# Kernel optimization log

Hardware: AMD Instinct MI355X
Metric: run time of the kernel (lower is better)

The kernel has to match this reference:

```python
import jax, jax.numpy as jnp
import numpy as np

B, S, F_IN = 8, 4096, 256      # batch, frames, mel bins
C = 256                        # model_complexity (out_features of attention)
G = 8                          # n_heads (groups)
K = 31                         # w_size (local window, odd)
F_OUT = 88                     # output_features (piano keys)
PAD = (K - 1) // 2


def setup_inputs() -> dict:
    key = jax.random.key(0)
    ks = jax.random.split(key, 7)
    s = 0.05
    return {
        "spec": jax.random.normal(ks[0], (B, S, F_IN), jnp.float32),
        "W_q": jax.random.normal(ks[1], (F_IN, C), jnp.float32) * s,
        "W_k": jax.random.normal(ks[2], (F_IN, C), jnp.float32) * s,
        "W_v": jax.random.normal(ks[3], (F_IN, C), jnp.float32) * s,
        "rel": jax.random.normal(ks[4], (C, K), jnp.float32),
        "W_lin": jax.random.normal(ks[5], (C, F_OUT), jnp.float32) * s,
        "b_lin": jax.random.normal(ks[6], (F_OUT,), jnp.float32) * s,
    }


def reference(spec, W_q, W_k, W_v, rel, W_lin, b_lin):
    b, s, _ = spec.shape
    d = C // G  # per-head dim
    # QKV projections (no bias, as in the module)
    q = spec @ W_q                                             # [B,S,C]
    padded = jnp.pad(spec, ((0, 0), (PAD, PAD), (0, 0)))       # [B,S+2p,F]
    k = padded @ W_k                                           # [B,S+2p,C]
    v = padded @ W_v
    # unfold: window index [S,K]
    idx = jnp.arange(s)[:, None] + jnp.arange(K)[None, :]      # [S,K]
    kw = jnp.transpose(k[:, idx, :], (0, 1, 3, 2))             # [B,S,C,K]
    vw = jnp.transpose(v[:, idx, :], (0, 1, 3, 2))             # [B,S,C,K]
    kw = kw + rel                                              # positional bias [C,K]
    kw = kw.reshape(b, s, G, d, K)
    vw = vw.reshape(b, s, G, d, K)
    qh = q.reshape(b, s, G, d)
    energy = jnp.einsum('bsgd,bsgdk->bsgk', qh, kw)            # [B,S,G,K]
    attn = jax.nn.softmax(energy, axis=-1)                     # [B,S,G,K]
    out = jnp.einsum('bsgk,bsgdk->bsgd', attn, vw).reshape(b, s, C)
    frame_pred = jax.nn.sigmoid(out @ W_lin + b_lin)           # [B,S,F_OUT]
    return frame_pred, attn
```

## Files before the change

kernel.cpp:

```cpp
#include <hip/hip_runtime.h>
#include <hip/hip_bf16.h>
#include <math.h>

#define B_   8
#define S_   4096
#define FIN  256
#define C_   256
#define G_   8
#define D_   32
#define K_   31
#define PAD_ 15
#define FOUT 88

typedef __bf16 bf16;
typedef __attribute__((ext_vector_type(8))) __bf16 bf16x8;
typedef __attribute__((ext_vector_type(4))) __bf16 bf16x4;
typedef __attribute__((ext_vector_type(4))) float f32x4;

#define MFMA16(A, B, C) __builtin_amdgcn_mfma_f32_16x16x32_bf16(A, B, C, 0, 0, 0)

__global__ __launch_bounds__(256) void split_spec(
    const float* __restrict__ spec, bf16* __restrict__ sh, bf16* __restrict__ sl)
{
    const size_t base = ((size_t)blockIdx.x * 256 + threadIdx.x) * 8;
    float4 x0 = *(const float4*)&spec[base];
    float4 x1 = *(const float4*)&spec[base + 4];
    float xs[8] = {x0.x, x0.y, x0.z, x0.w, x1.x, x1.y, x1.z, x1.w};
    bf16x8 H, L;
#pragma unroll
    for (int j = 0; j < 8; ++j) {
        bf16 h = (bf16)xs[j];
        H[j] = h;
        L[j] = (bf16)(xs[j] - (float)h);
    }
    *(bf16x8*)&sh[base] = H;
    *(bf16x8*)&sl[base] = L;
}

__global__ void split_w(const float* __restrict__ Wq, const float* __restrict__ Wk,
                        const float* __restrict__ Wv,
                        bf16* __restrict__ bth, bf16* __restrict__ btl)
{
    const int k = blockIdx.x;
    const int w = blockIdx.y;
    const int n = threadIdx.x;
    const float* W = (w == 0) ? Wq : (w == 1) ? Wk : Wv;
    float x = W[(size_t)k * 256 + n];
    bf16 h = (bf16)x;
    bf16 l = (bf16)(x - (float)h);
    size_t o = (size_t)w * 65536 + (size_t)n * 256 + k;
    bth[o] = h;
    btl[o] = l;
}

__global__ void split_wl(const float* __restrict__ Wl,
                         bf16* __restrict__ wlh, bf16* __restrict__ wll)
{
    const int k = blockIdx.x;
    const int n = threadIdx.x;
    const float x = (n < FOUT) ? Wl[(size_t)k * FOUT + n] : 0.f;
    bf16 h = (bf16)x;
    bf16 l = (bf16)(x - (float)h);
    wlh[(size_t)n * 256 + k] = h;
    wll[(size_t)n * 256 + k] = l;
}

__global__ void vt_pad(bf16* __restrict__ Vt) {
    const int idx = blockIdx.x * 256 + threadIdx.x;
    const int bd  = idx >> 4;
    const int pos = (idx & 15) * 4;
    const int off = (pos < 16) ? pos : 4096 + pos;
    bf16x4 z = {};
    *(bf16x4*)&Vt[(size_t)bd * 4160 + off] = z;
}

__global__ void rel_prep(const float* __restrict__ rel,
                         bf16* __restrict__ relH, bf16* __restrict__ relL) {
    const int idx = blockIdx.x * 256 + threadIdx.x;
    const int g = idx >> 10, k = (idx >> 5) & 31, d = idx & 31;
    const float v = (k < 31) ? rel[(size_t)(g * 32 + d) * 31 + k] : 0.f;
    bf16 h = (bf16)v;
    relH[idx] = h;
    relL[idx] = (bf16)(v - (float)h);
}

__device__ __forceinline__ void gload16(const bf16* g, bf16* l) {
    __builtin_amdgcn_global_load_lds(
        (const __attribute__((address_space(1))) void*)g,
        (__attribute__((address_space(3))) void*)l, 16, 0, 0);
}

__device__ __forceinline__ void stage_tile(const bf16* g, bf16* l, int t) {
    const int lg = ((t & 3) ^ ((t >> 3) & 3)) * 8;
    const int r0 = t >> 2;
    const int r1 = 64 + (t >> 2);
    const int u0 = (t & ~63) * 8;
    gload16(g + (size_t)r0 * 256 + lg, l + u0);
    gload16(g + (size_t)r1 * 256 + lg, l + u0 + 2048);
}

__device__ __forceinline__ bf16x8 frag_ld(const bf16* l, int r, int cl) {
    return *(const bf16x8*)&l[r * 32 + ((cl ^ ((r >> 1) & 3)) << 3)];
}

__global__ __launch_bounds__(256) void qkv_mfma(
    const bf16* __restrict__ sh, const bf16* __restrict__ sl,
    const bf16* __restrict__ bth, const bf16* __restrict__ btl,
    bf16* __restrict__ Qh, bf16* __restrict__ Ql,
    bf16* __restrict__ Kh, bf16* __restrict__ Kl,
    bf16* __restrict__ Vt)
{
    __shared__ bf16 lds[2 * 4 * 4096];

    const int t   = threadIdx.x;
    const int swz = ((blockIdx.x & 7) * 192) + (blockIdx.x >> 3);
    const int mt  = swz / 6, nt = swz % 6;
    const int wt  = nt >> 1;
    const int m0  = mt * 128, n0 = (nt & 1) * 128;
    const bool three = (wt < 2);

    const bf16* ah_g = sh  + (size_t)m0 * 256;
    const bf16* al_g = sl  + (size_t)m0 * 256;
    const bf16* bh_g = bth + (size_t)wt * 65536 + (size_t)n0 * 256;
    const bf16* bl_g = btl + (size_t)wt * 65536 + (size_t)n0 * 256;

    const int lane = t & 63, wid = t >> 6;
    const int wr = (wid >> 1) * 64, wc = (wid & 1) * 64;
    const int fr = lane & 15, cl = lane >> 4;

    f32x4 acc[4][4];
#pragma unroll
    for (int m = 0; m < 4; ++m)
#pragma unroll
        for (int n = 0; n < 4; ++n)
            acc[m][n] = (f32x4){0.f, 0.f, 0.f, 0.f};

    stage_tile(ah_g, lds, t);
    if (three) stage_tile(al_g, lds + 4096, t);
    stage_tile(bh_g, lds + 8192, t);
    stage_tile(bl_g, lds + 12288, t);
    __syncthreads();

    for (int ks = 0; ks < 8; ++ks) {
        const int cur = (ks & 1) * 16384;
        if (ks < 7) {
            const int nxt = 16384 - cur;
            const int ko  = (ks + 1) * 32;
            stage_tile(ah_g + ko, lds + nxt, t);
            if (three) stage_tile(al_g + ko, lds + nxt + 4096, t);
            stage_tile(bh_g + ko, lds + nxt + 8192, t);
            stage_tile(bl_g + ko, lds + nxt + 12288, t);
        }

        bf16x8 ah[4], bh[4], bl[4];
#pragma unroll
        for (int m = 0; m < 4; ++m) ah[m] = frag_ld(lds + cur, wr + m * 16 + fr, cl);
#pragma unroll
        for (int n = 0; n < 4; ++n) {
            bh[n] = frag_ld(lds + cur + 8192,  wc + n * 16 + fr, cl);
            bl[n] = frag_ld(lds + cur + 12288, wc + n * 16 + fr, cl);
        }
#pragma unroll
        for (int m = 0; m < 4; ++m)
#pragma unroll
            for (int n = 0; n < 4; ++n) {
                acc[m][n] = MFMA16(ah[m], bh[n], acc[m][n]);
                acc[m][n] = MFMA16(ah[m], bl[n], acc[m][n]);
            }
        if (three) {
            bf16x8 al[4];
#pragma unroll
            for (int m = 0; m < 4; ++m) al[m] = frag_ld(lds + cur + 4096, wr + m * 16 + fr, cl);
#pragma unroll
            for (int m = 0; m < 4; ++m)
#pragma unroll
                for (int n = 0; n < 4; ++n)
                    acc[m][n] = MFMA16(al[m], bh[n], acc[m][n]);
        }
        __syncthreads();
    }

    if (wt < 2) {
        bf16* Oh = (wt == 0) ? Qh : Kh;
        bf16* Ol = (wt == 0) ? Ql : Kl;
#pragma unroll
        for (int m = 0; m < 4; ++m) {
            const int gr = m0 + wr + m * 16 + cl * 4;
#pragma unroll
            for (int n = 0; n < 4; ++n) {
                const int gc = n0 + wc + n * 16 + fr;
#pragma unroll
                for (int i = 0; i < 4; ++i) {
                    const float v = acc[m][n][i];
                    const bf16 hh = (bf16)v;
                    const size_t off = (size_t)(gr + i) * 256 + gc;
                    Oh[off] = hh;
                    Ol[off] = (bf16)(v - (float)hh);
                }
            }
        }
    } else {
#pragma unroll
        for (int m = 0; m < 4; ++m) {
            const int gr = m0 + wr + m * 16 + cl * 4;
            const int bb = gr >> 12, sr = gr & 4095;
#pragma unroll
            for (int n = 0; n < 4; ++n) {
                const int gc = n0 + wc + n * 16 + fr;
                bf16x4 pk;
#pragma unroll
                for (int i = 0; i < 4; ++i) pk[i] = (bf16)acc[m][n][i];
                *(bf16x4*)&Vt[(size_t)(bb * 256 + gc) * 4160 + 16 + sr] = pk;
            }
        }
    }
}

__global__ __launch_bounds__(256) void attn_mfma(
    const bf16* __restrict__ Qh, const bf16* __restrict__ Ql,
    const bf16* __restrict__ Kh, const bf16* __restrict__ Kl,
    const bf16* __restrict__ Vt,
    const bf16* __restrict__ relH, const bf16* __restrict__ relL,
    float* __restrict__ attn, bf16* __restrict__ Obf)
{
    __shared__ char ldsb[18432];

    const int t    = threadIdx.x;
    const int wid  = t >> 6;
    const int lane = t & 63;
    const int fr   = lane & 15;
    const int q    = lane >> 4;
    const int f7   = fr & 7;
    const int sl   = lane >> 2;
    const int jj   = lane & 3;

    const int bid2 = ((blockIdx.x & 7) << 8) | (blockIdx.x >> 3);
    const int sg0  = bid2 << 4;
    const int b    = sg0 >> 12;
    const int s0   = sg0 & 4095;

    float* Rbuf = (float*)(ldsb + wid * 4608);
    float* Pf32 = Rbuf;
    bf16*  Pbuf = (bf16*) (ldsb + wid * 4608 + 2304);

    {
        uint* p32 = (uint*)Pbuf;
#pragma unroll
        for (int j = 0; j < 9; ++j) p32[lane + 64 * j] = 0u;
    }

    const size_t rowQ = (size_t)(sg0 + fr) * 256;

#pragma unroll
    for (int h = 0; h < 2; ++h) {
        asm volatile("" ::: "memory");
        const int g   = wid * 2 + h;
        const int dof = g * 32 + q * 8;

        const bf16x8 qh8 = *(const bf16x8*)&Qh[rowQ + dof];
        const bf16x8 ql8 = *(const bf16x8*)&Ql[rowQ + dof];

        f32x4 e0, e1, e2;
#pragma unroll
        for (int tau = 0; tau < 3; ++tau) {
            const int trel = s0 - 16 + tau * 16 + fr;
            bf16x8 kh8 = {}, kl8 = {};
            if ((unsigned)trel < 4096u) {
                const size_t rk = ((size_t)(b << 12) + trel) * 256 + dof;
                kh8 = *(const bf16x8*)&Kh[rk];
                kl8 = *(const bf16x8*)&Kl[rk];
            }
            f32x4 a = (f32x4){0.f, 0.f, 0.f, 0.f};
            a = MFMA16(kh8, qh8, a);
            a = MFMA16(kh8, ql8, a);
            a = MFMA16(kl8, qh8, a);
            if (tau == 0) e0 = a; else if (tau == 1) e1 = a; else e2 = a;
        }

#pragma unroll
        for (int kap = 0; kap < 2; ++kap) {
            const size_t ro = (size_t)(g * 32 + kap * 16 + fr) * 32 + q * 8;
            const bf16x8 rh8 = *(const bf16x8*)&relH[ro];
            const bf16x8 rl8 = *(const bf16x8*)&relL[ro];
            f32x4 rc = (f32x4){0.f, 0.f, 0.f, 0.f};
            rc = MFMA16(rh8, qh8, rc);
            rc = MFMA16(rh8, ql8, rc);
            rc = MFMA16(rl8, qh8, rc);
#pragma unroll
            for (int r = 0; r < 4; ++r)
                Rbuf[(kap * 16 + q * 4 + r) * 18 + fr] = rc[r];
        }

        float ev[3][4];
        float mx = -3.0e38f;
#pragma unroll
        for (int tau = 0; tau < 3; ++tau) {
#pragma unroll
            for (int r = 0; r < 4; ++r) {
                const int rp = q * 4 + r;
                const int kk = tau * 16 + rp - fr - 1;
                const float eb = (tau == 0) ? e0[r] : (tau == 1) ? e1[r] : e2[r];
                float v = eb + Rbuf[(kk & 31) * 18 + fr];
                const bool valid = (tau == 1) || ((tau == 0) ? (rp > fr) : (rp < fr));
                v = valid ? v : -3.0e38f;
                ev[tau][r] = v;
                mx = fmaxf(mx, v);
            }
        }
        mx = fmaxf(mx, __shfl_xor(mx, 16));
        mx = fmaxf(mx, __shfl_xor(mx, 32));
        float sum = 0.f;
#pragma unroll
        for (int tau = 0; tau < 3; ++tau)
#pragma unroll
            for (int r = 0; r < 4; ++r) {
                const float p = __expf(ev[tau][r] - mx);
                ev[tau][r] = p;
                sum += p;
            }
        sum += __shfl_xor(sum, 16);
        sum += __shfl_xor(sum, 32);
        const float inv = 1.f / sum;

#pragma unroll
        for (int tau = 0; tau < 3; ++tau)
#pragma unroll
            for (int r = 0; r < 4; ++r) {
                const int rp = q * 4 + r;
                const int kk = tau * 16 + rp - fr - 1;
                const bool valid = (tau == 1) || ((tau == 0) ? (rp > fr) : (rp < fr));
                if (valid) {
                    const float p = ev[tau][r] * inv;
                    Pf32[fr * 36 + kk] = p;
                    const int tl = tau * 16 + rp;
                    Pbuf[fr * 72 + (((tl >> 3) ^ f7) << 3) + (tl & 7)] = (bf16)p;
                }
            }

        asm volatile("" ::: "memory");
        {
            float* arow = &attn[((size_t)(sg0 + sl) * 8 + g) * 31];
#pragma unroll
            for (int i = 0; i < 8; ++i) {
                const int k = jj + 4 * i;
                if (k < 31) arow[k] = Pf32[sl * 36 + k];
            }
        }

        asm volatile("" ::: "memory");
        const bf16x8 a0 = *(const bf16x8*)&Pbuf[fr * 72 + ((q ^ f7) << 3)];
        const bf16x8 a1 = *(const bf16x8*)&Pbuf[fr * 72 + (((4 + q) ^ f7) << 3)];
#pragma unroll
        for (int dl = 0; dl < 2; ++dl) {
            const size_t vrow = (size_t)(b * 256 + g * 32 + dl * 16 + fr) * 4160
                              + s0 + q * 8;
            const bf16x8 v0 = *(const bf16x8*)&Vt[vrow];
            const bf16x8 v1 = *(const bf16x8*)&Vt[vrow + 32];
            f32x4 o = (f32x4){0.f, 0.f, 0.f, 0.f};
            o = MFMA16(v0, a0, o);
            o = MFMA16(v1, a1, o);
            bf16x4 pk;
#pragma unroll
            for (int r = 0; r < 4; ++r) pk[r] = (bf16)o[r];
            *(bf16x4*)&Obf[(size_t)(sg0 + fr) * 256 + g * 32 + dl * 16 + (q << 2)] = pk;
        }
    }
}

__global__ __launch_bounds__(256) void frame_mfma(
    const bf16* __restrict__ O,
    const bf16* __restrict__ wlh, const bf16* __restrict__ wll,
    const float* __restrict__ bl, float* __restrict__ frame)
{
    __shared__ bf16 lds[3 * 4096];

    const int t  = threadIdx.x;
    const int m0 = blockIdx.x * 128;

    const bf16* a_g = O + (size_t)m0 * 256;

    const int lane = t & 63, wid = t >> 6;
    const int wr = (wid >> 1) * 64, wc = (wid & 1) * 64;
    const int fr = lane & 15, cl = lane >> 4;

    f32x4 acc[4][4];
#pragma unroll
    for (int m = 0; m < 4; ++m)
#pragma unroll
        for (int n = 0; n < 4; ++n)
            acc[m][n] = (f32x4){0.f, 0.f, 0.f, 0.f};

    for (int ks = 0; ks < 8; ++ks) {
        const int ko = ks * 32;
        stage_tile(a_g + ko, lds, t);
        stage_tile(wlh + ko, lds + 4096, t);
        stage_tile(wll + ko, lds + 8192, t);
        __syncthreads();

        bf16x8 ah[4], bh[4], bl4[4];
#pragma unroll
        for (int m = 0; m < 4; ++m) ah[m] = frag_ld(lds, wr + m * 16 + fr, cl);
#pragma unroll
        for (int n = 0; n < 4; ++n) {
            bh[n]  = frag_ld(lds + 4096, wc + n * 16 + fr, cl);
            bl4[n] = frag_ld(lds + 8192, wc + n * 16 + fr, cl);
        }
#pragma unroll
        for (int m = 0; m < 4; ++m)
#pragma unroll
            for (int n = 0; n < 4; ++n) {
                acc[m][n] = MFMA16(ah[m], bh[n],  acc[m][n]);
                acc[m][n] = MFMA16(ah[m], bl4[n], acc[m][n]);
            }
        __syncthreads();
    }

#pragma unroll
    for (int m = 0; m < 4; ++m) {
        const int gr = m0 + wr + m * 16 + cl * 4;
#pragma unroll
        for (int n = 0; n < 4; ++n) {
            const int gc = wc + n * 16 + fr;
            if (gc < FOUT) {
                const float bb = bl[gc];
#pragma unroll
                for (int i = 0; i < 4; ++i) {
                    const float x = acc[m][n][i] + bb;
                    frame[(size_t)(gr + i) * FOUT + gc] = 1.f / (1.f + __expf(-x));
                }
            }
        }
    }
}

extern "C" void kernel_launch(void* const* d_in, const int* in_sizes, int n_in,
                              void* d_out, int out_size, void* d_ws, size_t ws_size,
                              hipStream_t stream) {
    (void)in_sizes; (void)n_in; (void)out_size; (void)ws_size;
    const float* spec = (const float*)d_in[0];
    const float* Wq   = (const float*)d_in[1];
    const float* Wk   = (const float*)d_in[2];
    const float* Wv   = (const float*)d_in[3];
    const float* rel  = (const float*)d_in[4];
    const float* Wl   = (const float*)d_in[5];
    const float* bl   = (const float*)d_in[6];

    float* frame = (float*)d_out;
    float* attn  = frame + (size_t)B_ * S_ * FOUT;

    bf16* sh   = (bf16*)d_out;
    bf16* sl   = sh + (size_t)B_ * S_ * FIN;
    bf16* bth  = (bf16*)((char*)d_out + 33554432);
    bf16* btl  = bth + 3 * 65536;
    bf16* relH = (bf16*)d_out;
    bf16* relL = relH + 8192;

    bf16* Qh  = (bf16*)d_ws;
    bf16* Ql  = Qh + (size_t)8388608;
    bf16* Kh  = Ql + (size_t)8388608;
    bf16* Kl  = Kh + (size_t)8388608;
    bf16* Vt  = Kl + (size_t)8388608;
    bf16* wlh = Vt + (size_t)8 * 256 * 4160;
    bf16* wll = wlh + 128 * 256;

    vt_pad    <<<dim3(128),     256, 0, stream>>>(Vt);
    split_spec<<<dim3(4096),    256, 0, stream>>>(spec, sh, sl);
    split_w   <<<dim3(256, 3),  256, 0, stream>>>(Wq, Wk, Wv, bth, btl);
    split_wl  <<<dim3(256),     128, 0, stream>>>(Wl, wlh, wll);
    qkv_mfma  <<<dim3(1536),    256, 0, stream>>>(sh, sl, bth, btl, Qh, Ql, Kh, Kl, Vt);
    rel_prep  <<<dim3(32),      256, 0, stream>>>(rel, relH, relL);
    attn_mfma <<<dim3(2048),    256, 0, stream>>>(Qh, Ql, Kh, Kl, Vt, relH, relL, attn, Qh);
    frame_mfma<<<dim3(256),     256, 0, stream>>>(Qh, wlh, wll, bl, frame);
}
```

Measured before the change: 128.5 us.

## Fuse spec bf16 split into QKV GEMM and merge prep kernels into one launch

The QKV GEMM now stages fp32 spec tiles straight into LDS with a swizzled layout and splits them into bf16 hi/lo in registers. This removes the separate split_spec pass and its intermediate bf16 buffers. The four small prep kernels (weight splits, Vt padding, rel prep) are merged into one block-dispatched kernel, cutting launches from eight to four. As a trade-off, the GEMM drops its double-buffered LDS pipeline for a single buffer with a sync every k-step. The fp32 A tile also doubles A's global and LDS traffic per tile, and the conversion is redone in every n-tile block.

```diff
diff --git a/kernel.cpp b/kernel.cpp
--- a/kernel.cpp
+++ b/kernel.cpp
@@ -19,72 +19,58 @@
 
 #define MFMA16(A, B, C) __builtin_amdgcn_mfma_f32_16x16x32_bf16(A, B, C, 0, 0, 0)
 
-__global__ __launch_bounds__(256) void split_spec(
-    const float* __restrict__ spec, bf16* __restrict__ sh, bf16* __restrict__ sl)
+__global__ __launch_bounds__(256) void prep_all(
+    const float* __restrict__ Wq, const float* __restrict__ Wk,
+    const float* __restrict__ Wv, const float* __restrict__ Wl,
+    const float* __restrict__ rel,
+    bf16* __restrict__ bth, bf16* __restrict__ btl,
+    bf16* __restrict__ wlh, bf16* __restrict__ wll,
+    bf16* __restrict__ Vt,
+    bf16* __restrict__ relH, bf16* __restrict__ relL)
 {
-    const size_t base = ((size_t)blockIdx.x * 256 + threadIdx.x) * 8;
-    float4 x0 = *(const float4*)&spec[base];
-    float4 x1 = *(const float4*)&spec[base + 4];
-    float xs[8] = {x0.x, x0.y, x0.z, x0.w, x1.x, x1.y, x1.z, x1.w};
-    bf16x8 H, L;
-#pragma unroll
-    for (int j = 0; j < 8; ++j) {
-        bf16 h = (bf16)xs[j];
-        H[j] = h;
-        L[j] = (bf16)(xs[j] - (float)h);
-    }
-    *(bf16x8*)&sh[base] = H;
-    *(bf16x8*)&sl[base] = L;
-}
-
-__global__ void split_w(const float* __restrict__ Wq, const float* __restrict__ Wk,
-                        const float* __restrict__ Wv,
-                        bf16* __restrict__ bth, bf16* __restrict__ btl)
-{
-    const int k = blockIdx.x;
-    const int w = blockIdx.y;
-    const int n = threadIdx.x;
-    const float* W = (w == 0) ? Wq : (w == 1) ? Wk : Wv;
-    float x = W[(size_t)k * 256 + n];
-    bf16 h = (bf16)x;
-    bf16 l = (bf16)(x - (float)h);
-    size_t o = (size_t)w * 65536 + (size_t)n * 256 + k;
-    bth[o] = h;
-    btl[o] = l;
-}
-
-__global__ void split_wl(const float* __restrict__ Wl,
-                         bf16* __restrict__ wlh, bf16* __restrict__ wll)
-{
-    const int k = blockIdx.x;
-    const int n = threadIdx.x;
-    const float x = (n < FOUT) ? Wl[(size_t)k * FOUT + n] : 0.f;
-    bf16 h = (bf16)x;
-    bf16 l = (bf16)(x - (float)h);
-    wlh[(size_t)n * 256 + k] = h;
-    wll[(size_t)n * 256 + k] = l;
-}
-
-__global__ void vt_pad(bf16* __restrict__ Vt) {
-    const int idx = blockIdx.x * 256 + threadIdx.x;
-    const int bd  = idx >> 4;
-    const int pos = (idx & 15) * 4;
-    const int off = (pos < 16) ? pos : 4096 + pos;
-    bf16x4 z = {};
-    *(bf16x4*)&Vt[(size_t)bd * 4160 + off] = z;
-}
-
-__global__ void rel_prep(const float* __restrict__ rel,
-                         bf16* __restrict__ relH, bf16* __restrict__ relL) {
-    const int idx = blockIdx.x * 256 + threadIdx.x;
-    const int g = idx >> 10, k = (idx >> 5) & 31, d = idx & 31;
-    const float v = (k < 31) ? rel[(size_t)(g * 32 + d) * 31 + k] : 0.f;
-    bf16 h = (bf16)v;
-    relH[idx] = h;
-    relL[idx] = (bf16)(v - (float)h);
+    const int bid = blockIdx.x;
+    const int t   = threadIdx.x;
+
+    if (bid < 768) {
+        const int w = bid >> 8;
+        const int k = bid & 255;
+        const float* W = (w == 0) ? Wq : (w == 1) ? Wk : Wv;
+        const float x = W[(size_t)k * 256 + t];
+        const bf16 h = (bf16)x;
+        const size_t o = (size_t)w * 65536 + (size_t)t * 256 + k;
+        bth[o] = h;
+        btl[o] = (bf16)(x - (float)h);
+    } else if (bid < 896) {
+        const int k = (bid - 768) * 2 + (t >> 7);
+        const int n = t & 127;
+        const float x = (n < FOUT) ? Wl[(size_t)k * FOUT + n] : 0.f;
+        const bf16 h = (bf16)x;
+        wlh[(size_t)n * 256 + k] = h;
+        wll[(size_t)n * 256 + k] = (bf16)(x - (float)h);
+    } else if (bid < 1024) {
+        const int idx = (bid - 896) * 256 + t;
+        const int bd  = idx >> 4;
+        const int pos = (idx & 15) * 4;
+        const int off = (pos < 16) ? pos : 4096 + pos;
+        bf16x4 z = {};
+        *(bf16x4*)&Vt[(size_t)bd * 4160 + off] = z;
+    } else {
+        const int idx = (bid - 1024) * 256 + t;
+        const int g = idx >> 10, k = (idx >> 5) & 31, d = idx & 31;
+        const float v = (k < 31) ? rel[(size_t)(g * 32 + d) * 31 + k] : 0.f;
+        const bf16 h = (bf16)v;
+        relH[idx] = h;
+        relL[idx] = (bf16)(v - (float)h);
+    }
 }
 
 __device__ __forceinline__ void gload16(const bf16* g, bf16* l) {
+    __builtin_amdgcn_global_load_lds(
+        (const __attribute__((address_space(1))) void*)g,
+        (__attribute__((address_space(3))) void*)l, 16, 0, 0);
+}
+
+__device__ __forceinline__ void gload16f(const float* g, float* l) {
     __builtin_amdgcn_global_load_lds(
         (const __attribute__((address_space(1))) void*)g,
         (__attribute__((address_space(3))) void*)l, 16, 0, 0);
@@ -103,14 +89,52 @@
     return *(const bf16x8*)&l[r * 32 + ((cl ^ ((r >> 1) & 3)) << 3)];
 }
 
+__device__ __forceinline__ void stage_tileA(const float* g, float* l, int t) {
+#pragma unroll
+    for (int i = 0; i < 4; ++i) {
+        const int li  = i * 256 + t;
+        const int row = li >> 3;
+        const int sc  = li & 7;
+        const int src = row * 256 + ((sc ^ (row & 7)) << 2);
+        gload16f(g + src, l + ((i << 8) + (t & ~63)) * 4);
+    }
+}
+
+__device__ __forceinline__ void frag_ldA(const float* A, int r, int cl,
+                                         bf16x8* hi, bf16x8* lo) {
+    const int base = r * 32;
+    const f32x4 a0 = *(const f32x4*)&A[base + ((( 2 * cl)     ^ (r & 7)) << 2)];
+    const f32x4 a1 = *(const f32x4*)&A[base + (((2 * cl + 1)  ^ (r & 7)) << 2)];
+    bf16x8 h, l;
+#pragma unroll
+    for (int j = 0; j < 4; ++j) {
+        const bf16 h0 = (bf16)a0[j]; h[j]     = h0; l[j]     = (bf16)(a0[j] - (float)h0);
+        const bf16 h1 = (bf16)a1[j]; h[4 + j] = h1; l[4 + j] = (bf16)(a1[j] - (float)h1);
+    }
+    *hi = h; *lo = l;
+}
+
+__device__ __forceinline__ bf16x8 frag_ldA_hi(const float* A, int r, int cl) {
+    const int base = r * 32;
+    const f32x4 a0 = *(const f32x4*)&A[base + ((( 2 * cl)     ^ (r & 7)) << 2)];
+    const f32x4 a1 = *(const f32x4*)&A[base + (((2 * cl + 1)  ^ (r & 7)) << 2)];
+    bf16x8 h;
+#pragma unroll
+    for (int j = 0; j < 4; ++j) { h[j] = (bf16)a0[j]; h[4 + j] = (bf16)a1[j]; }
+    return h;
+}
+
 __global__ __launch_bounds__(256) void qkv_mfma(
-    const bf16* __restrict__ sh, const bf16* __restrict__ sl,
+    const float* __restrict__ spec,
     const bf16* __restrict__ bth, const bf16* __restrict__ btl,
     bf16* __restrict__ Qh, bf16* __restrict__ Ql,
     bf16* __restrict__ Kh, bf16* __restrict__ Kl,
     bf16* __restrict__ Vt)
 {
-    __shared__ bf16 lds[2 * 4 * 4096];
+    __shared__ char ldsq[32768];
+    float* Af = (float*)ldsq;
+    bf16*  Bh = (bf16*)(ldsq + 16384);
+    bf16*  Bl = (bf16*)(ldsq + 24576);
 
     const int t   = threadIdx.x;
     const int swz = ((blockIdx.x & 7) * 192) + (blockIdx.x >> 3);
@@ -119,8 +143,7 @@
     const int m0  = mt * 128, n0 = (nt & 1) * 128;
     const bool three = (wt < 2);
 
-    const bf16* ah_g = sh  + (size_t)m0 * 256;
-    const bf16* al_g = sl  + (size_t)m0 * 256;
+    const float* a_g = spec + (size_t)m0 * 256;
     const bf16* bh_g = bth + (size_t)wt * 65536 + (size_t)n0 * 256;
     const bf16* bl_g = btl + (size_t)wt * 65536 + (size_t)n0 * 256;
 
@@ -135,47 +158,44 @@
         for (int n = 0; n < 4; ++n)
             acc[m][n] = (f32x4){0.f, 0.f, 0.f, 0.f};
 
-    stage_tile(ah_g, lds, t);
-    if (three) stage_tile(al_g, lds + 4096, t);
-    stage_tile(bh_g, lds + 8192, t);
-    stage_tile(bl_g, lds + 12288, t);
-    __syncthreads();
-
     for (int ks = 0; ks < 8; ++ks) {
-        const int cur = (ks & 1) * 16384;
-        if (ks < 7) {
-            const int nxt = 16384 - cur;
-            const int ko  = (ks + 1) * 32;
-            stage_tile(ah_g + ko, lds + nxt, t);
-            if (three) stage_tile(al_g + ko, lds + nxt + 4096, t);
-            stage_tile(bh_g + ko, lds + nxt + 8192, t);
-            stage_tile(bl_g + ko, lds + nxt + 12288, t);
-        }
-
-        bf16x8 ah[4], bh[4], bl[4];
-#pragma unroll
-        for (int m = 0; m < 4; ++m) ah[m] = frag_ld(lds + cur, wr + m * 16 + fr, cl);
+        const int ko = ks * 32;
+        stage_tileA(a_g + ko, Af, t);
+        stage_tile(bh_g + ko, Bh, t);
+        stage_tile(bl_g + ko, Bl, t);
+        __syncthreads();
+
+        bf16x8 bh8[4], bl8[4];
 #pragma unroll
         for (int n = 0; n < 4; ++n) {
-            bh[n] = frag_ld(lds + cur + 8192,  wc + n * 16 + fr, cl);
-            bl[n] = frag_ld(lds + cur + 12288, wc + n * 16 + fr, cl);
-        }
-#pragma unroll
-        for (int m = 0; m < 4; ++m)
-#pragma unroll
-            for (int n = 0; n < 4; ++n) {
-                acc[m][n] = MFMA16(ah[m], bh[n], acc[m][n]);
-                acc[m][n] = MFMA16(ah[m], bl[n], acc[m][n]);
-            }
+            bh8[n] = frag_ld(Bh, wc + n * 16 + fr, cl);
+            bl8[n] = frag_ld(Bl, wc + n * 16 + fr, cl);
+        }
         if (three) {
-            bf16x8 al[4];
-#pragma unroll
-            for (int m = 0; m < 4; ++m) al[m] = frag_ld(lds + cur + 4096, wr + m * 16 + fr, cl);
+            bf16x8 ahh[4], ahl[4];
 #pragma unroll
             for (int m = 0; m < 4; ++m)
-#pragma unroll
-                for (int n = 0; n < 4; ++n)
-                    acc[m][n] = MFMA16(al[m], bh[n], acc[m][n]);
+                frag_ldA(Af, wr + m * 16 + fr, cl, &ahh[m], &ahl[m]);
+#pragma unroll
+            for (int m = 0; m < 4; ++m)
+#pragma unroll
+                for (int n = 0; n < 4; ++n) {
+                    acc[m][n] = MFMA16(ahh[m], bh8[n], acc[m][n]);
+                    acc[m][n] = MFMA16(ahh[m], bl8[n], acc[m][n]);
+                    acc[m][n] = MFMA16(ahl[m], bh8[n], acc[m][n]);
+                }
+        } else {
+            bf16x8 ahh[4];
+#pragma unroll
+            for (int m = 0; m < 4; ++m)
+                ahh[m] = frag_ldA_hi(Af, wr + m * 16 + fr, cl);
+#pragma unroll
+            for (int m = 0; m < 4; ++m)
+#pragma unroll
+                for (int n = 0; n < 4; ++n) {
+                    acc[m][n] = MFMA16(ahh[m], bh8[n], acc[m][n]);
+                    acc[m][n] = MFMA16(ahh[m], bl8[n], acc[m][n]);
+                }
         }
         __syncthreads();
     }
@@ -448,8 +468,6 @@
     float* frame = (float*)d_out;
     float* attn  = frame + (size_t)B_ * S_ * FOUT;
 
-    bf16* sh   = (bf16*)d_out;
-    bf16* sl   = sh + (size_t)B_ * S_ * FIN;
     bf16* bth  = (bf16*)((char*)d_out + 33554432);
     bf16* btl  = bth + 3 * 65536;
     bf16* relH = (bf16*)d_out;
@@ -463,12 +481,9 @@
     bf16* wlh = Vt + (size_t)8 * 256 * 4160;
     bf16* wll = wlh + 128 * 256;
 
-    vt_pad    <<<dim3(128),     256, 0, stream>>>(Vt);
-    split_spec<<<dim3(4096),    256, 0, stream>>>(spec, sh, sl);
-    split_w   <<<dim3(256, 3),  256, 0, stream>>>(Wq, Wk, Wv, bth, btl);
-    split_wl  <<<dim3(256),     128, 0, stream>>>(Wl, wlh, wll);
-    qkv_mfma  <<<dim3(1536),    256, 0, stream>>>(sh, sl, bth, btl, Qh, Ql, Kh, Kl, Vt);
-    rel_prep  <<<dim3(32),      256, 0, stream>>>(rel, relH, relL);
-    attn_mfma <<<dim3(2048),    256, 0, stream>>>(Qh, Ql, Kh, Kl, Vt, relH, relL, attn, Qh);
-    frame_mfma<<<dim3(256),     256, 0, stream>>>(Qh, wlh, wll, bl, frame);
-}
+    prep_all  <<<dim3(1056), 256, 0, stream>>>(Wq, Wk, Wv, Wl, rel,
+                                               bth, btl, wlh, wll, Vt, relH, relL);
+    qkv_mfma  <<<dim3(1536), 256, 0, stream>>>(spec, bth, btl, Qh, Ql, Kh, Kl, Vt);
+    attn_mfma <<<dim3(2048), 256, 0, stream>>>(Qh, Ql, Kh, Kl, Vt, relH, relL, attn, Qh);
+    frame_mfma<<<dim3(256),  256, 0, stream>>>(Qh, wlh, wll, bl, frame);
+}
```

Result: faster. 116.7 us (-9.2%).
